# Optimization experiments

Measured on AMD Instinct MI355X. Metric: run time of the kernel, lower is better.

## Reference

```python
import jax, jax.numpy as jnp
import numpy as np

D_MODEL = 512
NHEAD = 8
HEAD_DIM = D_MODEL // NHEAD
DFF = 2048
RANK = 64
L = 1024
N = 8
EPS = 1e-5


def _layer_norm(x, g, b):
    m = jnp.mean(x, axis=-1, keepdims=True)
    v = jnp.mean(jnp.square(x - m), axis=-1, keepdims=True)
    return (x - m) * jax.lax.rsqrt(v + EPS) * g + b


def setup_inputs() -> dict:
    key = jax.random.key(0)
    ks = jax.random.split(key, 20)
    s = 1.0 / np.sqrt(D_MODEL)
    inp = {
        "q": jax.random.normal(ks[0], (L, N, D_MODEL), jnp.float32),
        "k": jax.random.normal(ks[1], (L, N, D_MODEL), jnp.float32),
        "v": jax.random.normal(ks[2], (L, N, D_MODEL), jnp.float32),
        # attention projections, stored (in, out) so x @ W
        "Wq": jax.random.normal(ks[3], (D_MODEL, D_MODEL), jnp.float32) * s,
        "bq": jnp.zeros((D_MODEL,), jnp.float32),
        "Wk": jax.random.normal(ks[4], (D_MODEL, D_MODEL), jnp.float32) * s,
        "bk": jnp.zeros((D_MODEL,), jnp.float32),
        "Wv": jax.random.normal(ks[5], (D_MODEL, D_MODEL), jnp.float32) * s,
        "bv": jnp.zeros((D_MODEL,), jnp.float32),
        "Wo": jax.random.normal(ks[6], (D_MODEL, D_MODEL), jnp.float32) * s,
        "bo": jnp.zeros((D_MODEL,), jnp.float32),
        "topk": jnp.float32(0.3),  # learned scalar, k = int(S * sigmoid(topk))
        "A1": jax.random.normal(ks[7], (D_MODEL, RANK), jnp.float32) * s,
        "B1": jax.random.normal(ks[8], (RANK, DFF), jnp.float32) / np.sqrt(RANK),
        "A2": jax.random.normal(ks[9], (DFF, RANK), jnp.float32) / np.sqrt(DFF),
        "B2": jax.random.normal(ks[10], (RANK, D_MODEL), jnp.float32) / np.sqrt(RANK),
        "g1": jnp.ones((D_MODEL,), jnp.float32),
        "be1": jnp.zeros((D_MODEL,), jnp.float32),
        "g2": jnp.ones((D_MODEL,), jnp.float32),
        "be2": jnp.zeros((D_MODEL,), jnp.float32),
    }
    return inp


def reference(q, k, v, Wq, bq, Wk, bk, Wv, bv, Wo, bo, topk,
              A1, B1, A2, B2, g1, be1, g2, be2):
    Lq, Nb, E = q.shape
    S = k.shape[0]
    H, Dh = NHEAD, HEAD_DIM

    # projections -> (N, L, H, Dh)
    qh = (q @ Wq + bq).reshape(Lq, Nb, H, Dh).transpose(1, 0, 2, 3)
    kh = (k @ Wk + bk).reshape(S, Nb, H, Dh).transpose(1, 0, 2, 3)
    vh = (v @ Wv + bv).reshape(S, Nb, H, Dh).transpose(1, 0, 2, 3)

    scores = jnp.einsum('nlhd,nshd->nlhs', qh, kh) / jnp.sqrt(jnp.float32(Dh))

    # dynamic top-k mask: keep the k = int(S * sigmoid(topk)) largest per row
    k_keep = (S * jax.nn.sigmoid(topk)).astype(jnp.int32)  # 588 for topk=0.3
    sorted_desc = jnp.sort(scores, axis=-1)[..., ::-1]
    idx = jnp.broadcast_to(k_keep - 1, scores.shape[:-1])[..., None]
    thresh = jnp.take_along_axis(sorted_desc, idx, axis=-1)  # k-th largest
    masked = jnp.where(scores >= thresh, scores, -jnp.inf)
    attn_w = jax.nn.softmax(masked, axis=-1)

    # note original flattens (d, h) order: 'nlhs,nshd->nldh' then view(L,N,E)
    ao = jnp.einsum('nlhs,nshd->nldh', attn_w, vh)
    ao = ao.transpose(1, 0, 2, 3).reshape(Lq, Nb, E)
    attn_out = ao @ Wo + bo

    src = _layer_norm(q + attn_out, g1, be1)
    ffn = jax.nn.relu(src @ A1 @ B1) @ A2 @ B2
    src = _layer_norm(src + ffn, g2, be2)
    return src
```

## Files before the change

### kernel.cpp

```cpp
#include <hip/hip_runtime.h>

typedef unsigned short u16;
typedef unsigned int u32;
using s16x8 = __attribute__((ext_vector_type(8))) short;
using s16x4 = __attribute__((ext_vector_type(4))) short;
using u16x4 = __attribute__((ext_vector_type(4))) unsigned short;
using u32x4 = __attribute__((ext_vector_type(4))) unsigned int;
using f32x4 = __attribute__((ext_vector_type(4))) float;

__device__ __forceinline__ u16 f2bf(float f) {
  unsigned int u = __float_as_uint(f);
  u += 0x7FFFu + ((u >> 16) & 1u);
  return (u16)(u >> 16);
}
__device__ __forceinline__ float bf2f(u16 b) {
  return __uint_as_float(((u32)b) << 16);
}
__device__ __forceinline__ u32 pkbf(float a, float b) {
  u32 r;
  asm("v_cvt_pk_bf16_f32 %0, %1, %2" : "=v"(r) : "v"(a), "v"(b));
  return r;
}
__device__ __forceinline__ u32 f2key(float f) {
  u32 u = __float_as_uint(f);
  u32 flip = (u32)((int)u >> 31) | 0x80000000u;
  return (u ^ flip) >> 16;
}
__device__ __forceinline__ float key2f(u32 k) {
  u32 t = k << 16;
  u32 msk = ((int)t < 0) ? 0x80000000u : 0xFFFF0000u;
  return __uint_as_float(t ^ msk);
}

__global__ __launch_bounds__(256) void prep_w(
    const float* __restrict__ Wq, const float* __restrict__ Wk, const float* __restrict__ Wv,
    const float* __restrict__ Wo, const float* __restrict__ A1, const float* __restrict__ B1,
    const float* __restrict__ A2, const float* __restrict__ B2,
    u16* __restrict__ WqT, u16* __restrict__ WkT, u16* __restrict__ WvT, u16* __restrict__ WoT,
    u16* __restrict__ A1T, u16* __restrict__ B1T, u16* __restrict__ A2T, u16* __restrict__ B2T) {
  int b = blockIdx.x, t = threadIdx.x;
  const float* src; u16* dst; int base, R, C;
  if (b < 1024)      { src = Wq; dst = WqT; base = 0;    R = 512;  C = 512; }
  else if (b < 2048) { src = Wk; dst = WkT; base = 1024; R = 512;  C = 512; }
  else if (b < 3072) { src = Wv; dst = WvT; base = 2048; R = 512;  C = 512; }
  else if (b < 4096) { src = Wo; dst = WoT; base = 3072; R = 512;  C = 512; }
  else if (b < 4224) { src = A1; dst = A1T; base = 4096; R = 512;  C = 64;  }
  else if (b < 4736) { src = B1; dst = B1T; base = 4224; R = 64;   C = 2048;}
  else if (b < 5248) { src = A2; dst = A2T; base = 4736; R = 2048; C = 64;  }
  else               { src = B2; dst = B2T; base = 5248; R = 64;   C = 512; }
  int idx = (b - base) * 256 + t;
  int r = idx / C, c = idx % C;
  dst[(size_t)c * R + r] = f2bf(src[idx]);
}

__global__ __launch_bounds__(256, 4) void qkv_fused(
    const float* __restrict__ q, const float* __restrict__ k, const float* __restrict__ v,
    const u16* __restrict__ WqT, const u16* __restrict__ WkT, const u16* __restrict__ WvT,
    const float* __restrict__ bq, const float* __restrict__ bk, const float* __restrict__ bv,
    u16* __restrict__ Qw, u16* __restrict__ Kw, u16* __restrict__ Vw) {
  __shared__ __align__(16) u16 As[128][72];
  __shared__ __align__(16) u16 Bs[128][72];
  const int z = blockIdx.z;
  const float* A = z == 0 ? q : (z == 1 ? k : v);
  const u16* Bt = z == 0 ? WqT : (z == 1 ? WkT : WvT);
  const float* bias = z == 0 ? bq : (z == 1 ? bk : bv);
  u16* outp = z == 0 ? Qw : (z == 1 ? Kw : Vw);

  const int tid = threadIdx.x;
  const int m0 = blockIdx.y * 128, n0 = blockIdx.x * 128;
  const int lane = tid & 63, wid = tid >> 6;
  const int l16 = lane & 15, hi = lane >> 4;
  const int wr = (wid >> 1) * 64, wc = (wid & 1) * 64;

  f32x4 acc[4][4];
#pragma unroll
  for (int i = 0; i < 4; ++i)
#pragma unroll
    for (int j = 0; j < 4; ++j) acc[i][j] = (f32x4){0.f, 0.f, 0.f, 0.f};

  for (int k0 = 0; k0 < 512; k0 += 64) {
    if (k0) __syncthreads();
#pragma unroll
    for (int i = 0; i < 4; ++i) {
      int idx = i * 256 + tid;
      int r = idx >> 3, cc = (idx & 7) * 8;
      float4 f0 = *(const float4*)&A[(size_t)(m0 + r) * 512 + k0 + cc];
      float4 f1 = *(const float4*)&A[(size_t)(m0 + r) * 512 + k0 + cc + 4];
      u32x4 pk;
      pk[0] = pkbf(f0.x, f0.y); pk[1] = pkbf(f0.z, f0.w);
      pk[2] = pkbf(f1.x, f1.y); pk[3] = pkbf(f1.z, f1.w);
      *(u32x4*)&As[r][cc] = pk;
      *(s16x8*)&Bs[r][cc] = *(const s16x8*)&Bt[(size_t)(n0 + r) * 512 + k0 + cc];
    }
    __syncthreads();
#pragma unroll
    for (int kk = 0; kk < 2; ++kk) {
      const int kb_ = kk * 32 + hi * 8;
      s16x8 af[4], bf[4];
#pragma unroll
      for (int mf = 0; mf < 4; ++mf) af[mf] = *(const s16x8*)&As[wr + mf * 16 + l16][kb_];
#pragma unroll
      for (int nf = 0; nf < 4; ++nf) bf[nf] = *(const s16x8*)&Bs[wc + nf * 16 + l16][kb_];
#pragma unroll
      for (int mf = 0; mf < 4; ++mf)
#pragma unroll
        for (int nf = 0; nf < 4; ++nf)
          acc[mf][nf] = __builtin_amdgcn_mfma_f32_16x16x32_bf16(af[mf], bf[nf], acc[mf][nf], 0, 0, 0);
    }
  }

#pragma unroll
  for (int mf = 0; mf < 4; ++mf)
#pragma unroll
    for (int nf = 0; nf < 4; ++nf)
#pragma unroll
      for (int i = 0; i < 4; ++i) {
        int row = m0 + wr + mf * 16 + hi * 4 + i;
        int col = n0 + wc + nf * 16 + l16;
        float val = acc[mf][nf][i] + bias[col];
        if (z == 0) val *= 0.125f;
        int l = row >> 3, n = row & 7, hh = col >> 6, d = col & 63;
        if (z < 2)
          outp[(((size_t)(n * 8 + hh) * 1024 + l) << 6) + d] = f2bf(val);
        else
          outp[((size_t)(n * 8 + hh) * 64 + d) * 1024 + l] = f2bf(val);
      }
}

__global__ __launch_bounds__(512, 4) void attn_kernel(const u16* __restrict__ Qw,
                                                      const u16* __restrict__ Kw,
                                                      const u16* __restrict__ Vw,
                                                      const float* __restrict__ topk,
                                                      u16* __restrict__ ao) {
  __shared__ __align__(16) u16 scb[32 * 1024];
  __shared__ __align__(16) u16 Qt[32][72];
  __shared__ float invs[32];
  const int tid = threadIdx.x, lane = tid & 63, wid = tid >> 6;
  const int l16 = lane & 15, hi = lane >> 4;
  const int mb = blockIdx.x, nh = blockIdx.y;

  const int kkeep = (int)(1024.f / (1.f + __expf(-topk[0])));

  {
    int r = tid >> 4, dc = (tid & 15) << 2;
    *(s16x4*)&Qt[r][dc] =
        *(const s16x4*)&Qw[((size_t)nh * 1024 + mb * 32 + r) * 64 + dc];
  }
  __syncthreads();

  {
    const u16* Kb = Kw + (size_t)nh * 1024 * 64;
    s16x8 bq0[2], bq1[2];
#pragma unroll
    for (int qh = 0; qh < 2; ++qh) {
      bq0[qh] = *(const s16x8*)&Qt[qh * 16 + l16][hi * 8];
      bq1[qh] = *(const s16x8*)&Qt[qh * 16 + l16][32 + hi * 8];
    }
    const int s0 = wid * 128;
#pragma unroll
    for (int nf = 0; nf < 8; ++nf) {
      const int sr = s0 + nf * 16 + l16;
      s16x8 a0 = *(const s16x8*)&Kb[(size_t)sr * 64 + hi * 8];
      s16x8 a1 = *(const s16x8*)&Kb[(size_t)sr * 64 + 32 + hi * 8];
#pragma unroll
      for (int qh = 0; qh < 2; ++qh) {
        f32x4 acc = {0.f, 0.f, 0.f, 0.f};
        acc = __builtin_amdgcn_mfma_f32_16x16x32_bf16(a0, bq0[qh], acc, 0, 0, 0);
        acc = __builtin_amdgcn_mfma_f32_16x16x32_bf16(a1, bq1[qh], acc, 0, 0, 0);
        const int row_q = qh * 16 + l16;
        u32 k0 = f2key(acc[0]) | (f2key(acc[1]) << 16);
        u32 k1 = f2key(acc[2]) | (f2key(acc[3]) << 16);
        char* rowq = (char*)scb + row_q * 2048;
        int boff = (2 * (s0 + nf * 16 + 4 * hi)) ^ ((row_q & 7) << 4);
        *(uint2*)(rowq + boff) = make_uint2(k0, k1);
      }
    }
  }
  __syncthreads();

  {
#pragma unroll
    for (int rp = 0; rp < 2; ++rp) {
      const int r0 = wid * 4 + rp * 2, r1 = r0 + 1;
      char* rb0 = (char*)scb + r0 * 2048;
      char* rb1 = (char*)scb + r1 * 2048;
      const int X0 = (r0 & 7) << 4, X1 = (r1 & 7) << 4;
      u32 ka[16], kb_[16];
#pragma unroll
      for (int c = 0; c < 8; ++c) {
        u32 wa = *(const u32*)(rb0 + ((4 * lane + 256 * c) ^ X0));
        u32 wb = *(const u32*)(rb1 + ((4 * lane + 256 * c) ^ X1));
        ka[2 * c] = wa & 0xFFFFu; ka[2 * c + 1] = wa >> 16;
        kb_[2 * c] = wb & 0xFFFFu; kb_[2 * c + 1] = wb >> 16;
      }
      u32 Ta = 0, Tb = 0;
#pragma unroll
      for (int bit = 15; bit >= 0; --bit) {
        u32 ca = Ta + (1u << bit), cb = Tb + (1u << bit);
        int na = 0, nb = 0;
#pragma unroll
        for (int j = 0; j < 16; ++j) {
          na += __popcll(__ballot(ka[j] >= ca));
          nb += __popcll(__ballot(kb_[j] >= cb));
        }
        if (na >= kkeep) Ta = ca;
        if (nb >= kkeep) Tb = cb;
      }
      const float tva = key2f(Ta), tvb = key2f(Tb);
      float suma = 0.f, sumb = 0.f;
#pragma unroll
      for (int c = 0; c < 8; ++c) {
        float ea0, ea1, eb0, eb1;
        {
          u32 kk0 = ka[2 * c], kk1 = ka[2 * c + 1];
          float v0 = key2f(kk0), v1 = key2f(kk1);
          ea0 = (kk0 >= Ta) ? __expf(v0 - tva) : 0.f;
          ea1 = (kk1 >= Ta) ? __expf(v1 - tva) : 0.f;
          suma += ea0 + ea1;
        }
        {
          u32 kk0 = kb_[2 * c], kk1 = kb_[2 * c + 1];
          float v0 = key2f(kk0), v1 = key2f(kk1);
          eb0 = (kk0 >= Tb) ? __expf(v0 - tvb) : 0.f;
          eb1 = (kk1 >= Tb) ? __expf(v1 - tvb) : 0.f;
          sumb += eb0 + eb1;
        }
        *(u32*)(rb0 + ((4 * lane + 256 * c) ^ X0)) = pkbf(ea0, ea1);
        *(u32*)(rb1 + ((4 * lane + 256 * c) ^ X1)) = pkbf(eb0, eb1);
      }
#pragma unroll
      for (int off = 1; off < 64; off <<= 1) {
        suma += __shfl_xor(suma, off);
        sumb += __shfl_xor(sumb, off);
      }
      if (lane == 0) {
        invs[r0] = __builtin_amdgcn_rcpf(suma);
        invs[r1] = __builtin_amdgcn_rcpf(sumb);
      }
    }
  }
  __syncthreads();

  {
    const u16* Vb = Vw + (size_t)nh * 64 * 1024;
    const int rh = wid >> 2, d0 = (wid & 3) * 16;
    f32x4 oacc0 = {0.f, 0.f, 0.f, 0.f};
    f32x4 oacc1 = {0.f, 0.f, 0.f, 0.f};
    const char* Pbase = (const char*)scb + (rh * 16 + l16) * 2048;
    const int Xp = (l16 & 7) << 4;
#pragma unroll
    for (int ks = 0; ks < 32; ks += 2) {
      int kb0 = (ks * 64 + hi * 16) ^ Xp;
      int kb1 = ((ks + 1) * 64 + hi * 16) ^ Xp;
      s16x8 a0 = *(const s16x8*)(Pbase + kb0);
      s16x8 a1 = *(const s16x8*)(Pbase + kb1);
      s16x8 b0 = *(const s16x8*)&Vb[(size_t)(d0 + l16) * 1024 + ks * 32 + hi * 8];
      s16x8 b1 = *(const s16x8*)&Vb[(size_t)(d0 + l16) * 1024 + (ks + 1) * 32 + hi * 8];
      oacc0 = __builtin_amdgcn_mfma_f32_16x16x32_bf16(a0, b0, oacc0, 0, 0, 0);
      oacc1 = __builtin_amdgcn_mfma_f32_16x16x32_bf16(a1, b1, oacc1, 0, 0, 0);
    }
    const int n = nh >> 3, hh = nh & 7;
#pragma unroll
    for (int i = 0; i < 4; ++i) {
      int l = mb * 32 + rh * 16 + hi * 4 + i;
      int d = d0 + l16;
      float vv = (oacc0[i] + oacc1[i]) * invs[rh * 16 + hi * 4 + i];
      ao[(size_t)(l * 8 + n) * 512 + d * 8 + hh] = f2bf(vv);
    }
  }
}

template <bool FIRST>
__global__ __launch_bounds__(256, 2) void gemm_ln(const u16* __restrict__ A,
                                                  const u16* __restrict__ Bt,
                                                  const float* __restrict__ bias,
                                                  const float* __restrict__ residf,
                                                  const u16* __restrict__ residb,
                                                  const float* __restrict__ g,
                                                  const float* __restrict__ be,
                                                  float* __restrict__ outf,
                                                  u16* __restrict__ outb) {
  constexpr int K = FIRST ? 512 : 64;
  __shared__ __align__(16) u16 As[16][72];
  __shared__ float red_s[4][16];
  __shared__ float red_q[4][16];
  const int tid = threadIdx.x;
  const int lane = tid & 63, wid = tid >> 6;
  const int l16 = lane & 15, hi = lane >> 4;
  const int m0 = blockIdx.x * 16;
  const int wc = wid * 128;

  f32x4 acc[8];
#pragma unroll
  for (int nf = 0; nf < 8; ++nf) acc[nf] = (f32x4){0.f, 0.f, 0.f, 0.f};

  for (int k0 = 0; k0 < K; k0 += 64) {
    if (k0) __syncthreads();
    {
      int r = tid >> 4, c = (tid & 15) << 2;
      *(s16x4*)&As[r][c] = *(const s16x4*)&A[(size_t)(m0 + r) * K + k0 + c];
    }
    __syncthreads();
#pragma unroll
    for (int kk = 0; kk < 2; ++kk) {
      const int kb_ = kk * 32 + hi * 8;
      s16x8 a = *(const s16x8*)&As[l16][kb_];
#pragma unroll
      for (int nf = 0; nf < 8; ++nf) {
        s16x8 b = *(const s16x8*)&Bt[(size_t)(wc + nf * 16 + l16) * K + k0 + kb_];
        acc[nf] = __builtin_amdgcn_mfma_f32_16x16x32_bf16(a, b, acc[nf], 0, 0, 0);
      }
    }
  }

#pragma unroll
  for (int nf = 0; nf < 8; ++nf) {
    int col = wc + nf * 16 + l16;
#pragma unroll
    for (int i = 0; i < 4; ++i) {
      float v = acc[nf][i];
      int row = m0 + hi * 4 + i;
      if (FIRST) v += bias[col] + residf[(size_t)row * 512 + col];
      else v += bf2f(residb[(size_t)row * 512 + col]);
      acc[nf][i] = v;
    }
  }
  float s[4] = {0.f, 0.f, 0.f, 0.f}, q2[4] = {0.f, 0.f, 0.f, 0.f};
#pragma unroll
  for (int nf = 0; nf < 8; ++nf)
#pragma unroll
    for (int i = 0; i < 4; ++i) {
      s[i] += acc[nf][i];
      q2[i] += acc[nf][i] * acc[nf][i];
    }
#pragma unroll
  for (int i = 0; i < 4; ++i) {
#pragma unroll
    for (int off = 1; off < 16; off <<= 1) {
      s[i] += __shfl_xor(s[i], off);
      q2[i] += __shfl_xor(q2[i], off);
    }
  }
  if (l16 == 0) {
#pragma unroll
    for (int i = 0; i < 4; ++i) {
      red_s[wid][hi * 4 + i] = s[i];
      red_q[wid][hi * 4 + i] = q2[i];
    }
  }
  __syncthreads();
  float mean[4], rstd[4];
#pragma unroll
  for (int i = 0; i < 4; ++i) {
    int r = hi * 4 + i;
    float ms = red_s[0][r] + red_s[1][r] + red_s[2][r] + red_s[3][r];
    float mq = red_q[0][r] + red_q[1][r] + red_q[2][r] + red_q[3][r];
    mean[i] = ms * (1.f / 512.f);
    float var = mq * (1.f / 512.f) - mean[i] * mean[i];
    rstd[i] = rsqrtf(var + 1e-5f);
  }
#pragma unroll
  for (int nf = 0; nf < 8; ++nf) {
    int col = wc + nf * 16 + l16;
    float gv = g[col], bev = be[col];
#pragma unroll
    for (int i = 0; i < 4; ++i) {
      int row = m0 + hi * 4 + i;
      float y = (acc[nf][i] - mean[i]) * rstd[i] * gv + bev;
      if (FIRST) outb[(size_t)row * 512 + col] = f2bf(y);
      else outf[(size_t)row * 512 + col] = y;
    }
  }
}

__global__ __launch_bounds__(256, 4) void ffn3(const u16* __restrict__ srcb,
                                               const u16* __restrict__ A1T,
                                               const u16* __restrict__ B1T,
                                               const u16* __restrict__ A2T,
                                               u16* __restrict__ w2) {
  __shared__ __align__(16) u16 As[32][72];
  __shared__ __align__(16) u16 Bs[64][72];
  __shared__ __align__(16) u16 Us[32][72];
  __shared__ __align__(16) u16 B1s[64][72];
  __shared__ __align__(16) u16 A2s[64][72];
  __shared__ __align__(16) u16 Hs[32][72];
  const int tid = threadIdx.x;
  const int lane = tid & 63, wid = tid >> 6;
  const int l16 = lane & 15, hi = lane >> 4;
  const int m0 = blockIdx.x * 32;
  const int wm = (wid & 1) * 16, wn = (wid >> 1) * 32;

  f32x4 accu[2];
  accu[0] = (f32x4){0.f, 0.f, 0.f, 0.f};
  accu[1] = (f32x4){0.f, 0.f, 0.f, 0.f};
  for (int k0 = 0; k0 < 512; k0 += 64) {
    if (k0) __syncthreads();
    {
      int r = tid >> 3, c = (tid & 7) << 3;
      *(s16x8*)&As[r][c] = *(const s16x8*)&srcb[(size_t)(m0 + r) * 512 + k0 + c];
    }
#pragma unroll
    for (int i = 0; i < 2; ++i) {
      int idx = i * 256 + tid;
      int r = idx >> 3, c = (idx & 7) << 3;
      *(s16x8*)&Bs[r][c] = *(const s16x8*)&A1T[(size_t)r * 512 + k0 + c];
    }
    __syncthreads();
#pragma unroll
    for (int kk = 0; kk < 2; ++kk) {
      const int kb_ = kk * 32 + hi * 8;
      s16x8 a = *(const s16x8*)&As[wm + l16][kb_];
#pragma unroll
      for (int j = 0; j < 2; ++j) {
        s16x8 b = *(const s16x8*)&Bs[wn + j * 16 + l16][kb_];
        accu[j] = __builtin_amdgcn_mfma_f32_16x16x32_bf16(a, b, accu[j], 0, 0, 0);
      }
    }
  }
  __syncthreads();
#pragma unroll
  for (int j = 0; j < 2; ++j)
#pragma unroll
    for (int i = 0; i < 4; ++i)
      Us[wm + hi * 4 + i][wn + j * 16 + l16] = f2bf(accu[j][i]);

  f32x4 w2a[2];
  w2a[0] = (f32x4){0.f, 0.f, 0.f, 0.f};
  w2a[1] = (f32x4){0.f, 0.f, 0.f, 0.f};
  for (int jc = 0; jc < 32; ++jc) {
#pragma unroll
    for (int i = 0; i < 2; ++i) {
      int idx = i * 256 + tid;
      int r = idx >> 3, c = (idx & 7) << 3;
      *(s16x8*)&B1s[r][c] = *(const s16x8*)&B1T[(size_t)(jc * 64 + r) * 64 + c];
      *(s16x8*)&A2s[r][c] = *(const s16x8*)&A2T[(size_t)r * 2048 + jc * 64 + c];
    }
    __syncthreads();
    f32x4 ha[2];
    ha[0] = (f32x4){0.f, 0.f, 0.f, 0.f};
    ha[1] = (f32x4){0.f, 0.f, 0.f, 0.f};
#pragma unroll
    for (int kk = 0; kk < 2; ++kk) {
      const int kb_ = kk * 32 + hi * 8;
      s16x8 a = *(const s16x8*)&Us[wm + l16][kb_];
#pragma unroll
      for (int j = 0; j < 2; ++j) {
        s16x8 b = *(const s16x8*)&B1s[wn + j * 16 + l16][kb_];
        ha[j] = __builtin_amdgcn_mfma_f32_16x16x32_bf16(a, b, ha[j], 0, 0, 0);
      }
    }
#pragma unroll
    for (int j = 0; j < 2; ++j)
#pragma unroll
      for (int i = 0; i < 4; ++i)
        Hs[wm + hi * 4 + i][wn + j * 16 + l16] = f2bf(fmaxf(ha[j][i], 0.f));
    __syncthreads();
#pragma unroll
    for (int kk = 0; kk < 2; ++kk) {
      const int kb_ = kk * 32 + hi * 8;
      s16x8 a = *(const s16x8*)&Hs[wm + l16][kb_];
#pragma unroll
      for (int j = 0; j < 2; ++j) {
        s16x8 b = *(const s16x8*)&A2s[wn + j * 16 + l16][kb_];
        w2a[j] = __builtin_amdgcn_mfma_f32_16x16x32_bf16(a, b, w2a[j], 0, 0, 0);
      }
    }
    __syncthreads();
  }
#pragma unroll
  for (int j = 0; j < 2; ++j)
#pragma unroll
    for (int i = 0; i < 4; ++i)
      w2[(size_t)(m0 + wm + hi * 4 + i) * 64 + wn + j * 16 + l16] = f2bf(w2a[j][i]);
}

extern "C" void kernel_launch(void* const* d_in, const int* in_sizes, int n_in,
                              void* d_out, int out_size, void* d_ws, size_t ws_size,
                              hipStream_t stream) {
  const float* q = (const float*)d_in[0];
  const float* k = (const float*)d_in[1];
  const float* v = (const float*)d_in[2];
  const float* Wq = (const float*)d_in[3];
  const float* bq = (const float*)d_in[4];
  const float* Wk = (const float*)d_in[5];
  const float* bk = (const float*)d_in[6];
  const float* Wv = (const float*)d_in[7];
  const float* bv = (const float*)d_in[8];
  const float* Wo = (const float*)d_in[9];
  const float* bo = (const float*)d_in[10];
  const float* topk = (const float*)d_in[11];
  const float* A1 = (const float*)d_in[12];
  const float* B1 = (const float*)d_in[13];
  const float* A2 = (const float*)d_in[14];
  const float* B2 = (const float*)d_in[15];
  const float* g1 = (const float*)d_in[16];
  const float* be1 = (const float*)d_in[17];
  const float* g2 = (const float*)d_in[18];
  const float* be2 = (const float*)d_in[19];

  char* ws = (char*)d_ws;
  constexpr size_t SZ_TOK_BF = (size_t)8192 * 512 * 2;
  constexpr size_t SZ_W_BF = (size_t)512 * 512 * 2;
  constexpr size_t O_QW = 0;
  constexpr size_t O_KW = O_QW + SZ_TOK_BF;
  constexpr size_t O_VW = O_KW + SZ_TOK_BF;
  constexpr size_t O_WQT = O_VW + SZ_TOK_BF;
  constexpr size_t O_WKT = O_WQT + SZ_W_BF;
  constexpr size_t O_WVT = O_WKT + SZ_W_BF;
  constexpr size_t O_WOT = O_WVT + SZ_W_BF;
  constexpr size_t O_A1T = O_WOT + SZ_W_BF;
  constexpr size_t O_B1T = O_A1T + 65536;
  constexpr size_t O_A2T = O_B1T + 262144;
  constexpr size_t O_B2T = O_A2T + 262144;
  constexpr size_t O_AO = O_B2T + 65536;
  constexpr size_t O_SRCB = O_AO + SZ_TOK_BF;
  constexpr size_t O_W2 = O_SRCB + SZ_TOK_BF;

  u16* Qw_ = (u16*)(ws + O_QW);
  u16* Kw_ = (u16*)(ws + O_KW);
  u16* Vw_ = (u16*)(ws + O_VW);
  u16* WqT = (u16*)(ws + O_WQT);
  u16* WkT = (u16*)(ws + O_WKT);
  u16* WvT = (u16*)(ws + O_WVT);
  u16* WoT = (u16*)(ws + O_WOT);
  u16* A1T = (u16*)(ws + O_A1T);
  u16* B1T = (u16*)(ws + O_B1T);
  u16* A2T = (u16*)(ws + O_A2T);
  u16* B2T = (u16*)(ws + O_B2T);
  u16* ao = (u16*)(ws + O_AO);
  u16* srcb = (u16*)(ws + O_SRCB);
  u16* w2 = (u16*)(ws + O_W2);

  prep_w<<<5376, 256, 0, stream>>>(Wq, Wk, Wv, Wo, A1, B1, A2, B2,
                                   WqT, WkT, WvT, WoT, A1T, B1T, A2T, B2T);

  qkv_fused<<<dim3(4, 64, 3), 256, 0, stream>>>(q, k, v, WqT, WkT, WvT,
                                                bq, bk, bv, Qw_, Kw_, Vw_);

  attn_kernel<<<dim3(32, 64), 512, 0, stream>>>(Qw_, Kw_, Vw_, topk, ao);

  gemm_ln<true><<<512, 256, 0, stream>>>(ao, WoT, bo, q, nullptr, g1, be1, nullptr, srcb);

  ffn3<<<256, 256, 0, stream>>>(srcb, A1T, B1T, A2T, w2);

  gemm_ln<false><<<512, 256, 0, stream>>>(w2, B2T, nullptr, nullptr, srcb, g2, be2,
                                          (float*)d_out, nullptr);
}
```

Measured before the change: 286.0 us.

## Tile weight transpose via LDS, fold log2e into Q scale, batch four top-k rows

The weight prep kernel now transposes 64x64 tiles through shared memory with float4 loads and vector stores, replacing the uncoalesced scattered per-element writes. The Q scale is multiplied by log2(e) so the softmax can use the native exp2 instruction instead of __expf. The top-k threshold search now handles four rows per wave at once instead of two pairs, giving more independent ballots per step at the cost of more registers. The bit loop is no longer explicitly unrolled.

```diff
diff --git a/kernel.cpp b/kernel.cpp
--- a/kernel.cpp
+++ b/kernel.cpp
@@ -38,19 +38,35 @@
     const float* __restrict__ A2, const float* __restrict__ B2,
     u16* __restrict__ WqT, u16* __restrict__ WkT, u16* __restrict__ WvT, u16* __restrict__ WoT,
     u16* __restrict__ A1T, u16* __restrict__ B1T, u16* __restrict__ A2T, u16* __restrict__ B2T) {
-  int b = blockIdx.x, t = threadIdx.x;
+  __shared__ u16 t[64][68];
+  int b = blockIdx.x, tid = threadIdx.x;
   const float* src; u16* dst; int base, R, C;
-  if (b < 1024)      { src = Wq; dst = WqT; base = 0;    R = 512;  C = 512; }
-  else if (b < 2048) { src = Wk; dst = WkT; base = 1024; R = 512;  C = 512; }
-  else if (b < 3072) { src = Wv; dst = WvT; base = 2048; R = 512;  C = 512; }
-  else if (b < 4096) { src = Wo; dst = WoT; base = 3072; R = 512;  C = 512; }
-  else if (b < 4224) { src = A1; dst = A1T; base = 4096; R = 512;  C = 64;  }
-  else if (b < 4736) { src = B1; dst = B1T; base = 4224; R = 64;   C = 2048;}
-  else if (b < 5248) { src = A2; dst = A2T; base = 4736; R = 2048; C = 64;  }
-  else               { src = B2; dst = B2T; base = 5248; R = 64;   C = 512; }
-  int idx = (b - base) * 256 + t;
-  int r = idx / C, c = idx % C;
-  dst[(size_t)c * R + r] = f2bf(src[idx]);
+  if (b < 64)        { src = Wq; dst = WqT; base = 0;   R = 512;  C = 512; }
+  else if (b < 128)  { src = Wk; dst = WkT; base = 64;  R = 512;  C = 512; }
+  else if (b < 192)  { src = Wv; dst = WvT; base = 128; R = 512;  C = 512; }
+  else if (b < 256)  { src = Wo; dst = WoT; base = 192; R = 512;  C = 512; }
+  else if (b < 264)  { src = A1; dst = A1T; base = 256; R = 512;  C = 64;  }
+  else if (b < 296)  { src = B1; dst = B1T; base = 264; R = 64;   C = 2048;}
+  else if (b < 328)  { src = A2; dst = A2T; base = 296; R = 2048; C = 64;  }
+  else               { src = B2; dst = B2T; base = 328; R = 64;   C = 512; }
+  int ti = b - base;
+  int tpr = C >> 6;
+  int r0 = (ti / tpr) * 64, c0 = (ti % tpr) * 64;
+#pragma unroll
+  for (int i = 0; i < 4; ++i) {
+    int r = i * 16 + (tid >> 4), c = (tid & 15) * 4;
+    float4 f = *(const float4*)&src[(size_t)(r0 + r) * C + c0 + c];
+    t[r][c] = f2bf(f.x); t[r][c + 1] = f2bf(f.y);
+    t[r][c + 2] = f2bf(f.z); t[r][c + 3] = f2bf(f.w);
+  }
+  __syncthreads();
+#pragma unroll
+  for (int i = 0; i < 4; ++i) {
+    int cc = i * 16 + (tid >> 4), rr = (tid & 15) * 4;
+    u16x4 o;
+    o[0] = t[rr][cc]; o[1] = t[rr + 1][cc]; o[2] = t[rr + 2][cc]; o[3] = t[rr + 3][cc];
+    *(u16x4*)&dst[(size_t)(c0 + cc) * R + r0 + rr] = o;
+  }
 }
 
 __global__ __launch_bounds__(256, 4) void qkv_fused(
@@ -118,7 +134,7 @@
         int row = m0 + wr + mf * 16 + hi * 4 + i;
         int col = n0 + wc + nf * 16 + l16;
         float val = acc[mf][nf][i] + bias[col];
-        if (z == 0) val *= 0.125f;
+        if (z == 0) val *= 0.18033688f;
         int l = row >> 3, n = row & 7, hh = col >> 6, d = col & 63;
         if (z < 2)
           outp[(((size_t)(n * 8 + hh) * 1024 + l) << 6) + d] = f2bf(val);
@@ -179,64 +195,87 @@
   __syncthreads();
 
   {
-#pragma unroll
-    for (int rp = 0; rp < 2; ++rp) {
-      const int r0 = wid * 4 + rp * 2, r1 = r0 + 1;
-      char* rb0 = (char*)scb + r0 * 2048;
-      char* rb1 = (char*)scb + r1 * 2048;
-      const int X0 = (r0 & 7) << 4, X1 = (r1 & 7) << 4;
-      u32 ka[16], kb_[16];
-#pragma unroll
-      for (int c = 0; c < 8; ++c) {
-        u32 wa = *(const u32*)(rb0 + ((4 * lane + 256 * c) ^ X0));
-        u32 wb = *(const u32*)(rb1 + ((4 * lane + 256 * c) ^ X1));
-        ka[2 * c] = wa & 0xFFFFu; ka[2 * c + 1] = wa >> 16;
-        kb_[2 * c] = wb & 0xFFFFu; kb_[2 * c + 1] = wb >> 16;
-      }
-      u32 Ta = 0, Tb = 0;
-#pragma unroll
-      for (int bit = 15; bit >= 0; --bit) {
-        u32 ca = Ta + (1u << bit), cb = Tb + (1u << bit);
-        int na = 0, nb = 0;
-#pragma unroll
-        for (int j = 0; j < 16; ++j) {
-          na += __popcll(__ballot(ka[j] >= ca));
-          nb += __popcll(__ballot(kb_[j] >= cb));
-        }
-        if (na >= kkeep) Ta = ca;
-        if (nb >= kkeep) Tb = cb;
-      }
-      const float tva = key2f(Ta), tvb = key2f(Tb);
-      float suma = 0.f, sumb = 0.f;
-#pragma unroll
-      for (int c = 0; c < 8; ++c) {
-        float ea0, ea1, eb0, eb1;
-        {
-          u32 kk0 = ka[2 * c], kk1 = ka[2 * c + 1];
-          float v0 = key2f(kk0), v1 = key2f(kk1);
-          ea0 = (kk0 >= Ta) ? __expf(v0 - tva) : 0.f;
-          ea1 = (kk1 >= Ta) ? __expf(v1 - tva) : 0.f;
-          suma += ea0 + ea1;
-        }
-        {
-          u32 kk0 = kb_[2 * c], kk1 = kb_[2 * c + 1];
-          float v0 = key2f(kk0), v1 = key2f(kk1);
-          eb0 = (kk0 >= Tb) ? __expf(v0 - tvb) : 0.f;
-          eb1 = (kk1 >= Tb) ? __expf(v1 - tvb) : 0.f;
-          sumb += eb0 + eb1;
-        }
-        *(u32*)(rb0 + ((4 * lane + 256 * c) ^ X0)) = pkbf(ea0, ea1);
-        *(u32*)(rb1 + ((4 * lane + 256 * c) ^ X1)) = pkbf(eb0, eb1);
-      }
-#pragma unroll
-      for (int off = 1; off < 64; off <<= 1) {
-        suma += __shfl_xor(suma, off);
-        sumb += __shfl_xor(sumb, off);
-      }
-      if (lane == 0) {
-        invs[r0] = __builtin_amdgcn_rcpf(suma);
-        invs[r1] = __builtin_amdgcn_rcpf(sumb);
-      }
+    const int r = wid * 4;
+    char* rb0 = (char*)scb + (r + 0) * 2048;
+    char* rb1 = (char*)scb + (r + 1) * 2048;
+    char* rb2 = (char*)scb + (r + 2) * 2048;
+    char* rb3 = (char*)scb + (r + 3) * 2048;
+    const int X0 = ((r + 0) & 7) << 4, X1 = ((r + 1) & 7) << 4;
+    const int X2 = ((r + 2) & 7) << 4, X3 = ((r + 3) & 7) << 4;
+    u32 k0a[16], k1a[16], k2a[16], k3a[16];
+#pragma unroll
+    for (int c = 0; c < 8; ++c) {
+      u32 w0 = *(const u32*)(rb0 + ((4 * lane + 256 * c) ^ X0));
+      u32 w1 = *(const u32*)(rb1 + ((4 * lane + 256 * c) ^ X1));
+      u32 w2 = *(const u32*)(rb2 + ((4 * lane + 256 * c) ^ X2));
+      u32 w3 = *(const u32*)(rb3 + ((4 * lane + 256 * c) ^ X3));
+      k0a[2 * c] = w0 & 0xFFFFu; k0a[2 * c + 1] = w0 >> 16;
+      k1a[2 * c] = w1 & 0xFFFFu; k1a[2 * c + 1] = w1 >> 16;
+      k2a[2 * c] = w2 & 0xFFFFu; k2a[2 * c + 1] = w2 >> 16;
+      k3a[2 * c] = w3 & 0xFFFFu; k3a[2 * c + 1] = w3 >> 16;
+    }
+    u32 T0 = 0, T1 = 0, T2 = 0, T3 = 0;
+    for (int bit = 15; bit >= 0; --bit) {
+      const u32 bb = 1u << bit;
+      u32 c0 = T0 + bb, c1 = T1 + bb, c2 = T2 + bb, c3 = T3 + bb;
+      int n0 = 0, n1 = 0, n2 = 0, n3 = 0;
+#pragma unroll
+      for (int j = 0; j < 16; ++j) {
+        n0 += __popcll(__ballot(k0a[j] >= c0));
+        n1 += __popcll(__ballot(k1a[j] >= c1));
+        n2 += __popcll(__ballot(k2a[j] >= c2));
+        n3 += __popcll(__ballot(k3a[j] >= c3));
+      }
+      T0 = (n0 >= kkeep) ? c0 : T0;
+      T1 = (n1 >= kkeep) ? c1 : T1;
+      T2 = (n2 >= kkeep) ? c2 : T2;
+      T3 = (n3 >= kkeep) ? c3 : T3;
+    }
+    const float tv0 = key2f(T0), tv1 = key2f(T1), tv2 = key2f(T2), tv3 = key2f(T3);
+    float s0 = 0.f, s1 = 0.f, s2 = 0.f, s3 = 0.f;
+#pragma unroll
+    for (int c = 0; c < 8; ++c) {
+      {
+        u32 ka = k0a[2 * c], kb = k0a[2 * c + 1];
+        float e0 = (ka >= T0) ? __builtin_amdgcn_exp2f(key2f(ka) - tv0) : 0.f;
+        float e1 = (kb >= T0) ? __builtin_amdgcn_exp2f(key2f(kb) - tv0) : 0.f;
+        s0 += e0 + e1;
+        *(u32*)(rb0 + ((4 * lane + 256 * c) ^ X0)) = pkbf(e0, e1);
+      }
+      {
+        u32 ka = k1a[2 * c], kb = k1a[2 * c + 1];
+        float e0 = (ka >= T1) ? __builtin_amdgcn_exp2f(key2f(ka) - tv1) : 0.f;
+        float e1 = (kb >= T1) ? __builtin_amdgcn_exp2f(key2f(kb) - tv1) : 0.f;
+        s1 += e0 + e1;
+        *(u32*)(rb1 + ((4 * lane + 256 * c) ^ X1)) = pkbf(e0, e1);
+      }
+      {
+        u32 ka = k2a[2 * c], kb = k2a[2 * c + 1];
+        float e0 = (ka >= T2) ? __builtin_amdgcn_exp2f(key2f(ka) - tv2) : 0.f;
+        float e1 = (kb >= T2) ? __builtin_amdgcn_exp2f(key2f(kb) - tv2) : 0.f;
+        s2 += e0 + e1;
+        *(u32*)(rb2 + ((4 * lane + 256 * c) ^ X2)) = pkbf(e0, e1);
+      }
+      {
+        u32 ka = k3a[2 * c], kb = k3a[2 * c + 1];
+        float e0 = (ka >= T3) ? __builtin_amdgcn_exp2f(key2f(ka) - tv3) : 0.f;
+        float e1 = (kb >= T3) ? __builtin_amdgcn_exp2f(key2f(kb) - tv3) : 0.f;
+        s3 += e0 + e1;
+        *(u32*)(rb3 + ((4 * lane + 256 * c) ^ X3)) = pkbf(e0, e1);
+      }
+    }
+#pragma unroll
+    for (int off = 1; off < 64; off <<= 1) {
+      s0 += __shfl_xor(s0, off);
+      s1 += __shfl_xor(s1, off);
+      s2 += __shfl_xor(s2, off);
+      s3 += __shfl_xor(s3, off);
+    }
+    if (lane == 0) {
+      invs[r + 0] = __builtin_amdgcn_rcpf(s0);
+      invs[r + 1] = __builtin_amdgcn_rcpf(s1);
+      invs[r + 2] = __builtin_amdgcn_rcpf(s2);
+      invs[r + 3] = __builtin_amdgcn_rcpf(s3);
     }
   }
   __syncthreads();
@@ -531,8 +570,8 @@
   u16* srcb = (u16*)(ws + O_SRCB);
   u16* w2 = (u16*)(ws + O_W2);
 
-  prep_w<<<5376, 256, 0, stream>>>(Wq, Wk, Wv, Wo, A1, B1, A2, B2,
-                                   WqT, WkT, WvT, WoT, A1T, B1T, A2T, B2T);
+  prep_w<<<336, 256, 0, stream>>>(Wq, Wk, Wv, Wo, A1, B1, A2, B2,
+                                  WqT, WkT, WvT, WoT, A1T, B1T, A2T, B2T);
 
   qkv_fused<<<dim3(4, 64, 3), 256, 0, stream>>>(q, k, v, WqT, WkT, WvT,
                                                 bq, bk, bv, Qw_, Kw_, Vw_);
```

Result: no change. 286.6 us (+0.2%).
